# Kernel optimization log

Hardware: AMD Instinct MI355X
Metric: run time of the kernel (lower is better)

Reference implementation:

```python
import jax, jax.numpy as jnp
import numpy as np

B, HW, N = 4, 65536, 48
NEAR, FAR = 0.1, 10.0


def setup_inputs() -> dict:
    key = jax.random.key(0)
    k1, k2, k3 = jax.random.split(key, 3)
    rgb = jax.random.uniform(k1, (B, HW, N, 3), dtype=jnp.float32)
    sigma = jax.random.uniform(k2, (B, HW, N, 1), dtype=jnp.float32)
    # sorted sample depths in [near, far] along each ray
    z = jax.random.uniform(k3, (B, HW, N), dtype=jnp.float32)
    z_vals = NEAR + (FAR - NEAR) * jnp.sort(z, axis=-1)
    return {"rgb": rgb, "sigma": sigma, "z_vals": z_vals}


def reference(rgb, sigma, z_vals):
    # distances between consecutive samples; last dist is a huge cap value
    dists = z_vals[..., 1:] - z_vals[..., :-1]                       # (B, HW, N-1)
    dists = jnp.concatenate(
        [dists, jnp.full_like(dists[..., :1], 1e10)], axis=-1)      # (B, HW, N)
    alpha = 1.0 - jnp.exp(-sigma[..., 0] * dists)                    # (B, HW, N)
    # transmittance: exclusive cumulative product of (1 - alpha)
    T = jnp.cumprod(1.0 - alpha + 1e-10, axis=-1)
    T = jnp.concatenate([jnp.ones_like(T[..., :1]), T[..., :-1]], axis=-1)
    weights = alpha * T                                              # (B, HW, N)
    rgb_map = jnp.einsum('bns,bnsc->bnc', weights, rgb)              # (B, HW, 3)
    depth_map = jnp.sum(weights * z_vals, axis=-1)                   # (B, HW)
    return rgb_map, depth_map
```

## Files before the change

### kernel.cpp

```cpp
#include <hip/hip_runtime.h>

#define N_SAMP 48

__global__ __launch_bounds__(256) void volrender_kernel(
    const float4* __restrict__ rgb4,
    const float4* __restrict__ sigma4,
    const float4* __restrict__ z4,
    float* __restrict__ out_rgb,
    float* __restrict__ out_depth,
    int n_rays)
{
    int ray = blockIdx.x * blockDim.x + threadIdx.x;
    if (ray >= n_rays) return;

    float zv[N_SAMP];
    float4* zvv = reinterpret_cast<float4*>(zv);
#pragma unroll
    for (int k = 0; k < N_SAMP / 4; ++k)
        zvv[k] = z4[(size_t)ray * (N_SAMP / 4) + k];

    float T = 1.0f;
    float ar = 0.0f, ag = 0.0f, ab = 0.0f, ad = 0.0f;

#pragma unroll
    for (int g = 0; g < N_SAMP / 4; ++g) {
        float4 sg = sigma4[(size_t)ray * (N_SAMP / 4) + g];
        float4 r0 = rgb4[(size_t)ray * 36 + g * 3 + 0];
        float4 r1 = rgb4[(size_t)ray * 36 + g * 3 + 1];
        float4 r2 = rgb4[(size_t)ray * 36 + g * 3 + 2];
        float sig[4] = {sg.x, sg.y, sg.z, sg.w};
        float rr[12] = {r0.x, r0.y, r0.z, r0.w,
                        r1.x, r1.y, r1.z, r1.w,
                        r2.x, r2.y, r2.z, r2.w};
#pragma unroll
        for (int j = 0; j < 4; ++j) {
            const int i = g * 4 + j;
            float dist  = (i == N_SAMP - 1) ? 1e10f : (zv[i + 1] - zv[i]);
            float alpha = 1.0f - __expf(-sig[j] * dist);
            float w     = alpha * T;
            T *= (1.0f - alpha + 1e-10f);
            ar = fmaf(w, rr[j * 3 + 0], ar);
            ag = fmaf(w, rr[j * 3 + 1], ag);
            ab = fmaf(w, rr[j * 3 + 2], ab);
            ad = fmaf(w, zv[i], ad);
        }
    }

    out_rgb[(size_t)ray * 3 + 0] = ar;
    out_rgb[(size_t)ray * 3 + 1] = ag;
    out_rgb[(size_t)ray * 3 + 2] = ab;
    out_depth[ray] = ad;
}

extern "C" void kernel_launch(void* const* d_in, const int* in_sizes, int n_in,
                              void* d_out, int out_size, void* d_ws, size_t ws_size,
                              hipStream_t stream) {
    const float4* rgb4   = (const float4*)d_in[0];
    const float4* sigma4 = (const float4*)d_in[1];
    const float4* z4     = (const float4*)d_in[2];

    const int n_rays = in_sizes[2] / N_SAMP;

    float* out_rgb   = (float*)d_out;
    float* out_depth = out_rgb + (size_t)n_rays * 3;

    const int block = 256;
    const int grid  = (n_rays + block - 1) / block;
    hipLaunchKernelGGL(volrender_kernel, dim3(grid), dim3(block), 0, stream,
                       rgb4, sigma4, z4, out_rgb, out_depth, n_rays);
}
```

Before: 329.8 us.

## Split each ray across four threads with shuffle-based transmittance scan

Each ray is now handled by four lanes, each covering 12 consecutive samples. Every lane computes its local weighted sums and its transmittance product. The lanes then combine the earlier segments' products through shuffles and reduce the four partial results with xor-shuffles. This gives four times as many threads and makes the per-thread loads more contiguous across neighbouring lanes, aimed at better memory coalescing and latency hiding in this bandwidth-bound kernel. In exchange it adds shuffle overhead, an extra scalar z load, and a small change in floating-point association.

```diff
diff --git a/kernel.cpp b/kernel.cpp
--- a/kernel.cpp
+++ b/kernel.cpp
@@ -1,55 +1,83 @@
 #include <hip/hip_runtime.h>
 
 #define N_SAMP 48
+#define TPR 4
+#define SPT (N_SAMP / TPR)
 
 __global__ __launch_bounds__(256) void volrender_kernel(
     const float4* __restrict__ rgb4,
     const float4* __restrict__ sigma4,
     const float4* __restrict__ z4,
+    const float*  __restrict__ zf,
     float* __restrict__ out_rgb,
     float* __restrict__ out_depth,
     int n_rays)
 {
-    int ray = blockIdx.x * blockDim.x + threadIdx.x;
+    const int tid = blockIdx.x * blockDim.x + threadIdx.x;
+    const int ray = tid >> 2;
+    const int q   = tid & 3;
     if (ray >= n_rays) return;
 
-    float zv[N_SAMP];
-    float4* zvv = reinterpret_cast<float4*>(zv);
+    float zloc[SPT];
+    float4* zv = reinterpret_cast<float4*>(zloc);
+    const size_t zbase = (size_t)ray * 12 + q * 3;
 #pragma unroll
-    for (int k = 0; k < N_SAMP / 4; ++k)
-        zvv[k] = z4[(size_t)ray * (N_SAMP / 4) + k];
+    for (int k = 0; k < 3; ++k) zv[k] = z4[zbase + k];
+
+    float znext = 0.0f;
+    if (q < 3) znext = zf[(size_t)ray * N_SAMP + q * SPT + SPT];
+
+    float sloc[SPT];
+    float4* sv = reinterpret_cast<float4*>(sloc);
+#pragma unroll
+    for (int k = 0; k < 3; ++k) sv[k] = sigma4[zbase + k];
+
+    float rloc[SPT * 3];
+    float4* rv = reinterpret_cast<float4*>(rloc);
+    const size_t rbase = (size_t)ray * 36 + q * 9;
+#pragma unroll
+    for (int k = 0; k < 9; ++k) rv[k] = rgb4[rbase + k];
 
     float T = 1.0f;
     float ar = 0.0f, ag = 0.0f, ab = 0.0f, ad = 0.0f;
-
 #pragma unroll
-    for (int g = 0; g < N_SAMP / 4; ++g) {
-        float4 sg = sigma4[(size_t)ray * (N_SAMP / 4) + g];
-        float4 r0 = rgb4[(size_t)ray * 36 + g * 3 + 0];
-        float4 r1 = rgb4[(size_t)ray * 36 + g * 3 + 1];
-        float4 r2 = rgb4[(size_t)ray * 36 + g * 3 + 2];
-        float sig[4] = {sg.x, sg.y, sg.z, sg.w};
-        float rr[12] = {r0.x, r0.y, r0.z, r0.w,
-                        r1.x, r1.y, r1.z, r1.w,
-                        r2.x, r2.y, r2.z, r2.w};
-#pragma unroll
-        for (int j = 0; j < 4; ++j) {
-            const int i = g * 4 + j;
-            float dist  = (i == N_SAMP - 1) ? 1e10f : (zv[i + 1] - zv[i]);
-            float alpha = 1.0f - __expf(-sig[j] * dist);
-            float w     = alpha * T;
-            T *= (1.0f - alpha + 1e-10f);
-            ar = fmaf(w, rr[j * 3 + 0], ar);
-            ag = fmaf(w, rr[j * 3 + 1], ag);
-            ab = fmaf(w, rr[j * 3 + 2], ab);
-            ad = fmaf(w, zv[i], ad);
-        }
+    for (int j = 0; j < SPT; ++j) {
+        const float zn   = (j < SPT - 1) ? zloc[j + 1] : znext;
+        const bool  last = (j == SPT - 1);
+        float dist  = (last && q == TPR - 1) ? 1e10f : (zn - zloc[j]);
+        float alpha = 1.0f - __expf(-sloc[j] * dist);
+        float w     = alpha * T;
+        T *= (1.0f - alpha + 1e-10f);
+        ar = fmaf(w, rloc[3 * j + 0], ar);
+        ag = fmaf(w, rloc[3 * j + 1], ag);
+        ab = fmaf(w, rloc[3 * j + 2], ab);
+        ad = fmaf(w, zloc[j], ad);
     }
 
-    out_rgb[(size_t)ray * 3 + 0] = ar;
-    out_rgb[(size_t)ray * 3 + 1] = ag;
-    out_rgb[(size_t)ray * 3 + 2] = ab;
-    out_depth[ray] = ad;
+    const int lane = threadIdx.x & 63;
+    const int base = lane & ~3;
+    const float P  = T;
+    const float P0 = __shfl(P, base + 0);
+    const float P1 = __shfl(P, base + 1);
+    const float P2 = __shfl(P, base + 2);
+    float Tpre = 1.0f;
+    if (q > 0) Tpre *= P0;
+    if (q > 1) Tpre *= P1;
+    if (q > 2) Tpre *= P2;
+
+    ar *= Tpre; ag *= Tpre; ab *= Tpre; ad *= Tpre;
+
+    ar += __shfl_xor(ar, 1); ag += __shfl_xor(ag, 1);
+    ab += __shfl_xor(ab, 1); ad += __shfl_xor(ad, 1);
+    ar += __shfl_xor(ar, 2); ag += __shfl_xor(ag, 2);
+    ab += __shfl_xor(ab, 2); ad += __shfl_xor(ad, 2);
+
+    if (q == 0) {
+        out_rgb[(size_t)ray * 3 + 0] = ar;
+        out_rgb[(size_t)ray * 3 + 1] = ag;
+        out_rgb[(size_t)ray * 3 + 2] = ab;
+        out_depth[ray] = ad;
+    }
 }
 
 extern "C" void kernel_launch(void* const* d_in, const int* in_sizes, int n_in,
@@ -58,14 +86,16 @@
     const float4* rgb4   = (const float4*)d_in[0];
     const float4* sigma4 = (const float4*)d_in[1];
     const float4* z4     = (const float4*)d_in[2];
+    const float*  zf     = (const float*)d_in[2];
 
     const int n_rays = in_sizes[2] / N_SAMP;
 
     float* out_rgb   = (float*)d_out;
     float* out_depth = out_rgb + (size_t)n_rays * 3;
 
-    const int block = 256;
-    const int grid  = (n_rays + block - 1) / block;
+    const int block     = 256;
+    const int n_threads = n_rays * TPR;
+    const int grid      = (n_threads + block - 1) / block;
     hipLaunchKernelGGL(volrender_kernel, dim3(grid), dim3(block), 0, stream,
-                       rgb4, sigma4, z4, out_rgb, out_depth, n_rays);
+                       rgb4, sigma4, z4, zf, out_rgb, out_depth, n_rays);
 }
```

After: 282.1 us. -14.4%, faster.

## Stage ray data through LDS with coalesced loads and split rays across 16 lanes

Applied to the files above, without the earlier changes.

Replaces the one-thread-per-ray kernel, whose per-thread loads are widely strided and poorly coalesced, with a grid-stride kernel. Each block stages 16 rays of rgb, sigma and z into LDS using fully coalesced float4 loads. Each ray is then split across 16 lanes of 3 samples each, combined with a shuffle prefix-product of transmittance and an xor-shuffle reduction. The cost is extra LDS traffic, block barriers, shuffle work, and a small numerical reordering of the transmittance product.

```diff
diff --git a/kernel.cpp b/kernel.cpp
--- a/kernel.cpp
+++ b/kernel.cpp
@@ -1,55 +1,123 @@
 #include <hip/hip_runtime.h>
 
 #define N_SAMP 48
+#define RPC    16
+#define BLOCK  256
+#define TPR    16
+#define SPT    3
 
-__global__ __launch_bounds__(256) void volrender_kernel(
+#define RGB_F4   (RPC * 36)
+#define SIG_F4   (RPC * 12)
+#define Z_F4     (RPC * 12)
+#define SIG_OFF  (RPC * 144)
+#define Z_OFF    (SIG_OFF + RPC * 48)
+#define LDS_FLOATS (Z_OFF + RPC * 48)
+
+__global__ __launch_bounds__(BLOCK, 8) void volrender_kernel(
     const float4* __restrict__ rgb4,
     const float4* __restrict__ sigma4,
     const float4* __restrict__ z4,
     float* __restrict__ out_rgb,
     float* __restrict__ out_depth,
-    int n_rays)
+    int n_rays, int n_chunks)
 {
-    int ray = blockIdx.x * blockDim.x + threadIdx.x;
-    if (ray >= n_rays) return;
+    __shared__ float bf[LDS_FLOATS];
+    float4* bf4 = reinterpret_cast<float4*>(bf);
 
-    float zv[N_SAMP];
-    float4* zvv = reinterpret_cast<float4*>(zv);
+    const int t   = threadIdx.x;
+    const int rl  = t >> 4;
+    const int sub = t & 15;
+
+    const size_t rgb_tot = (size_t)n_rays * 36;
+    const size_t sz_tot  = (size_t)n_rays * 12;
+
+    for (int chunk = blockIdx.x; chunk < n_chunks; chunk += gridDim.x) {
+        const size_t ray0 = (size_t)chunk * RPC;
+
+        if (chunk != blockIdx.x) __syncthreads();
+
+        {
+            const size_t rb = ray0 * 36;
+            const size_t zb = ray0 * 12;
+            float4 a0 = make_float4(0, 0, 0, 0), a1 = a0, a2 = a0, sg = a0, zv = a0;
+            if (rb + t       < rgb_tot) a0 = rgb4[rb + t];
+            if (rb + 256 + t < rgb_tot) a1 = rgb4[rb + 256 + t];
+            if (t < RGB_F4 - 512 && rb + 512 + t < rgb_tot) a2 = rgb4[rb + 512 + t];
+            if (t < SIG_F4 && zb + t < sz_tot) sg = sigma4[zb + t];
+            if (t < Z_F4   && zb + t < sz_tot) zv = z4[zb + t];
+            bf4[t]       = a0;
+            bf4[256 + t] = a1;
+            if (t < RGB_F4 - 512) bf4[512 + t] = a2;
+            if (t < SIG_F4) bf4[SIG_OFF / 4 + t] = sg;
+            if (t < Z_F4)   bf4[Z_OFF / 4 + t]   = zv;
+        }
+        __syncthreads();
+
+        const int zbase = Z_OFF + rl * 48 + sub * 3;
+        const float zl0 = bf[zbase + 0];
+        const float zl1 = bf[zbase + 1];
+        const float zl2 = bf[zbase + 2];
+        const float z3  = (sub == 15) ? 0.0f : bf[zbase + 3];
+
+        const int sbase = SIG_OFF + rl * 48 + sub * 3;
+        const float s0 = bf[sbase + 0];
+        const float s1 = bf[sbase + 1];
+        const float s2 = bf[sbase + 2];
+
+        const int rbase = rl * 144 + sub * 9;
+        float r[9];
 #pragma unroll
-    for (int k = 0; k < N_SAMP / 4; ++k)
-        zvv[k] = z4[(size_t)ray * (N_SAMP / 4) + k];
+        for (int k = 0; k < 9; ++k) r[k] = bf[rbase + k];
 
-    float T = 1.0f;
-    float ar = 0.0f, ag = 0.0f, ab = 0.0f, ad = 0.0f;
+        float T = 1.0f, ar = 0.0f, ag = 0.0f, ab = 0.0f, ad = 0.0f;
+        {
+            float alpha = 1.0f - __expf(-s0 * (zl1 - zl0));
+            float w = alpha * T; T *= (1.0f - alpha + 1e-10f);
+            ar = fmaf(w, r[0], ar); ag = fmaf(w, r[1], ag);
+            ab = fmaf(w, r[2], ab); ad = fmaf(w, zl0, ad);
+        }
+        {
+            float alpha = 1.0f - __expf(-s1 * (zl2 - zl1));
+            float w = alpha * T; T *= (1.0f - alpha + 1e-10f);
+            ar = fmaf(w, r[3], ar); ag = fmaf(w, r[4], ag);
+            ab = fmaf(w, r[5], ab); ad = fmaf(w, zl1, ad);
+        }
+        {
+            float dist  = (sub == 15) ? 1e10f : (z3 - zl2);
+            float alpha = 1.0f - __expf(-s2 * dist);
+            float w = alpha * T; T *= (1.0f - alpha + 1e-10f);
+            ar = fmaf(w, r[6], ar); ag = fmaf(w, r[7], ag);
+            ab = fmaf(w, r[8], ab); ad = fmaf(w, zl2, ad);
+        }
+
+        float x = T;
+#pragma unroll
+        for (int d = 1; d < 16; d <<= 1) {
+            float v = __shfl_up(x, (unsigned)d, 16);
+            if (sub >= d) x *= v;
+        }
+        float e = __shfl_up(x, 1u, 16);
+        if (sub == 0) e = 1.0f;
+        ar *= e; ag *= e; ab *= e; ad *= e;
 
 #pragma unroll
-    for (int g = 0; g < N_SAMP / 4; ++g) {
-        float4 sg = sigma4[(size_t)ray * (N_SAMP / 4) + g];
-        float4 r0 = rgb4[(size_t)ray * 36 + g * 3 + 0];
-        float4 r1 = rgb4[(size_t)ray * 36 + g * 3 + 1];
-        float4 r2 = rgb4[(size_t)ray * 36 + g * 3 + 2];
-        float sig[4] = {sg.x, sg.y, sg.z, sg.w};
-        float rr[12] = {r0.x, r0.y, r0.z, r0.w,
-                        r1.x, r1.y, r1.z, r1.w,
-                        r2.x, r2.y, r2.z, r2.w};
-#pragma unroll
-        for (int j = 0; j < 4; ++j) {
-            const int i = g * 4 + j;
-            float dist  = (i == N_SAMP - 1) ? 1e10f : (zv[i + 1] - zv[i]);
-            float alpha = 1.0f - __expf(-sig[j] * dist);
-            float w     = alpha * T;
-            T *= (1.0f - alpha + 1e-10f);
-            ar = fmaf(w, rr[j * 3 + 0], ar);
-            ag = fmaf(w, rr[j * 3 + 1], ag);
-            ab = fmaf(w, rr[j * 3 + 2], ab);
-            ad = fmaf(w, zv[i], ad);
+        for (int d = 1; d < 16; d <<= 1) {
+            ar += __shfl_xor(ar, d);
+            ag += __shfl_xor(ag, d);
+            ab += __shfl_xor(ab, d);
+            ad += __shfl_xor(ad, d);
+        }
+
+        if (sub == 0) {
+            const size_t ray = ray0 + rl;
+            if (ray < (size_t)n_rays) {
+                out_rgb[ray * 3 + 0] = ar;
+                out_rgb[ray * 3 + 1] = ag;
+                out_rgb[ray * 3 + 2] = ab;
+                out_depth[ray] = ad;
+            }
         }
     }
-
-    out_rgb[(size_t)ray * 3 + 0] = ar;
-    out_rgb[(size_t)ray * 3 + 1] = ag;
-    out_rgb[(size_t)ray * 3 + 2] = ab;
-    out_depth[ray] = ad;
 }
 
 extern "C" void kernel_launch(void* const* d_in, const int* in_sizes, int n_in,
@@ -59,13 +127,14 @@
     const float4* sigma4 = (const float4*)d_in[1];
     const float4* z4     = (const float4*)d_in[2];
 
-    const int n_rays = in_sizes[2] / N_SAMP;
+    const int n_rays   = in_sizes[2] / N_SAMP;
+    const int n_chunks = (n_rays + RPC - 1) / RPC;
 
     float* out_rgb   = (float*)d_out;
     float* out_depth = out_rgb + (size_t)n_rays * 3;
 
-    const int block = 256;
-    const int grid  = (n_rays + block - 1) / block;
-    hipLaunchKernelGGL(volrender_kernel, dim3(grid), dim3(block), 0, stream,
-                       rgb4, sigma4, z4, out_rgb, out_depth, n_rays);
+    int grid = 2048;
+    if (grid > n_chunks) grid = n_chunks;
+    hipLaunchKernelGGL(volrender_kernel, dim3(grid), dim3(BLOCK), 0, stream,
+                       rgb4, sigma4, z4, out_rgb, out_depth, n_rays, n_chunks);
 }
```

New measurement: 281.3 us. -14.7%, faster.
